# Kernel tuning notes

Hardware: AMD Instinct MI355X
Metric: run time of the kernel (lower is better)

Reference implementation:

```python
import jax, jax.numpy as jnp
import numpy as np
import math

N_HEADS = 8

def setup_inputs() -> dict:
    key = jax.random.key(0)
    ks = jax.random.split(key, 5)
    B, S, D = 2, 2048, 512
    return {
        "x": jax.random.normal(ks[0], (B, S, D), dtype=jnp.float32),
        "w_in": jax.random.normal(ks[1], (3 * D, D), dtype=jnp.float32) * (1.0 / math.sqrt(D)),
        "b_in": jax.random.normal(ks[2], (3 * D,), dtype=jnp.float32) * 0.01,
        "w_out": jax.random.normal(ks[3], (D, D), dtype=jnp.float32) * (1.0 / math.sqrt(D)),
        "b_out": jax.random.normal(ks[4], (D,), dtype=jnp.float32) * 0.01,
        "casual_mask": 1,
    }

def reference(x, w_in, b_in, w_out, b_out, casual_mask):
    B, S, D = x.shape
    H = N_HEADS
    dh = D // H
    # in_proj: torch Linear -> x @ W.T + b
    qvk = x @ w_in.T + b_in  # [B, S, 3D]
    # NOTE: source unpacks as q, v, k (chunk order quirk preserved)
    q, v, k = jnp.split(qvk, 3, axis=-1)
    # [B, S, D] -> [B, H, S, dh]
    def to_heads(t):
        return t.reshape(B, S, H, dh).transpose(0, 2, 1, 3)
    q, k, v = to_heads(q), to_heads(k), to_heads(v)
    scores = jnp.einsum("bhqd,bhkd->bhqk", q, k)  # [B, H, S, S]
    if casual_mask:
        # mask BEFORE scaling, as in the source (-inf unaffected by division)
        tri = jnp.triu(jnp.ones((S, S), dtype=bool), k=1)
        scores = jnp.where(tri, -jnp.inf, scores)
    scores = scores / math.sqrt(dh)
    attn = jax.nn.softmax(scores, axis=-1)
    out = jnp.einsum("bhqk,bhkd->bhqd", attn, v)  # [B, H, S, dh]
    out = out.transpose(0, 2, 1, 3).reshape(B, S, D)
    return out @ w_out.T + b_out
```

## Files before the change

### kernel.cpp

```cpp
#include <hip/hip_runtime.h>
#include <hip/hip_bf16.h>

typedef unsigned short u16;
typedef unsigned int u32;
typedef __attribute__((ext_vector_type(8))) short bf16x8;
typedef __attribute__((ext_vector_type(4))) short bf16x4;
typedef __attribute__((ext_vector_type(4))) float f32x4;

#define DEVI __device__ __forceinline__

DEVI u16 f2bf(float f) {
  union { float f; unsigned int u; } v; v.f = f;
  unsigned int u = v.u;
  unsigned int r = (u + 0x7fffu + ((u >> 16) & 1u)) >> 16;
  return (u16)r;
}

DEVI float bf2f(u16 b) {
  union { unsigned int u; float f; } v; v.u = ((unsigned int)b) << 16;
  return v.f;
}

DEVI float fexp2(float x) {
#if __has_builtin(__builtin_amdgcn_exp2f)
  return __builtin_amdgcn_exp2f(x);
#else
  return exp2f(x);
#endif
}

DEVI u32 pkbf(float a, float b) {
  union { float f; u32 u; } ua, ub;
  ua.f = a; ub.f = b;
  return __builtin_amdgcn_perm(ua.u + 0x8000u, ub.u + 0x8000u, 0x07060302u);
}

DEVI void lds_cp16(u16* lds, const u16* g) {
  __builtin_amdgcn_global_load_lds(
      (const __attribute__((address_space(1))) u32*)g,
      (__attribute__((address_space(3))) u32*)lds, 16, 0, 0);
}

DEVI f32x4 mfma16x16x16_bf16(bf16x4 a, bf16x4 b, f32x4 c) {
#if __has_builtin(__builtin_amdgcn_mfma_f32_16x16x16bf16_1k)
  return __builtin_amdgcn_mfma_f32_16x16x16bf16_1k(a, b, c, 0, 0, 0);
#else
  f32x4 d;
  asm volatile("v_mfma_f32_16x16x16_bf16 %0, %1, %2, %3"
               : "=v"(d) : "v"(a), "v"(b), "v"(c));
  return d;
#endif
}

__global__ __launch_bounds__(256) void cvt_all(
    const float4* __restrict__ x, const float4* __restrict__ wi,
    const float4* __restrict__ wo, u16* __restrict__ xb,
    u16* __restrict__ wib, u16* __restrict__ wob) {
  int i = blockIdx.x * 256 + threadIdx.x;
  const float4* src; u16* dst; int off;
  if (i < 524288)      { src = x;  dst = xb;  off = i; }
  else if (i < 720896) { src = wi; dst = wib; off = i - 524288; }
  else                 { src = wo; dst = wob; off = i - 720896; }
  float4 f = src[off];
  ushort4 o;
  o.x = f2bf(f.x); o.y = f2bf(f.y); o.z = f2bf(f.z); o.w = f2bf(f.w);
  ((ushort4*)dst)[off] = o;
}

__global__ __launch_bounds__(256) void inproj_gemm(
    const u16* __restrict__ xb, const u16* __restrict__ wb,
    const float* __restrict__ bin,
    u16* __restrict__ Qb, u16* __restrict__ Kb, u16* __restrict__ Vt) {
  const int K = 512;
  const float SCL = 0.180336878f;
  __shared__ u16 At[2][128 * 32];
  __shared__ u16 Bt[2][128 * 32];
  int tid = threadIdx.x;
  int w = tid >> 6, lane = tid & 63;
  int ql = lane & 15, quad = lane >> 4;
  int wr = w >> 1, wc = w & 1;
  int mtile = blockIdx.x * 128, ntile = blockIdx.y * 128;

  int r4 = lane >> 2, c4 = lane & 3;
  int swz4 = c4 ^ (r4 & 3);

  const u16* ag0 = xb + (size_t)(mtile + w * 32 + r4) * K + swz4 * 8;
  const u16* bg0 = wb + (size_t)(ntile + w * 32 + r4) * K + swz4 * 8;

  f32x4 acc[4][4];
#pragma unroll
  for (int t = 0; t < 4; ++t)
#pragma unroll
    for (int u = 0; u < 4; ++u) acc[t][u] = (f32x4){0, 0, 0, 0};

  lds_cp16(&At[0][w * 1024], ag0);
  lds_cp16(&At[0][w * 1024 + 512], ag0 + 16 * K);
  lds_cp16(&Bt[0][w * 1024], bg0);
  lds_cp16(&Bt[0][w * 1024 + 512], bg0 + 16 * K);

  int cb = ql & 3;
  for (int kk = 0; kk < 16; ++kk) {
    int cur = kk & 1;
    __syncthreads();
    if (kk < 15) {
      int k0 = (kk + 1) * 32;
      lds_cp16(&At[cur ^ 1][w * 1024], ag0 + k0);
      lds_cp16(&At[cur ^ 1][w * 1024 + 512], ag0 + 16 * K + k0);
      lds_cp16(&Bt[cur ^ 1][w * 1024], bg0 + k0);
      lds_cp16(&Bt[cur ^ 1][w * 1024 + 512], bg0 + 16 * K + k0);
    }
    bf16x8 af[4], bf[4];
#pragma unroll
    for (int t = 0; t < 4; ++t) {
      int row = wr * 64 + t * 16 + ql;
      af[t] = *(const bf16x8*)(&At[cur][row * 32 + ((quad ^ cb) * 8)]);
    }
#pragma unroll
    for (int u = 0; u < 4; ++u) {
      int row = wc * 64 + u * 16 + ql;
      bf[u] = *(const bf16x8*)(&Bt[cur][row * 32 + ((quad ^ cb) * 8)]);
    }
#pragma unroll
    for (int t = 0; t < 4; ++t)
#pragma unroll
      for (int u = 0; u < 4; ++u)
        acc[t][u] = __builtin_amdgcn_mfma_f32_16x16x32_bf16(af[t], bf[u], acc[t][u], 0, 0, 0);
  }

#pragma unroll
  for (int u = 0; u < 4; ++u) {
    int n = ntile + wc * 64 + u * 16 + ql;
    float bias = bin[n];
    int chunk = n >> 9;
    int nc = n & 511;
    int h = nc >> 6, d = nc & 63;
#pragma unroll
    for (int t = 0; t < 4; ++t)
#pragma unroll
      for (int r = 0; r < 4; ++r) {
        int m = mtile + wr * 64 + t * 16 + quad * 4 + r;
        int b = m >> 11, s = m & 2047;
        float v = acc[t][u][r] + bias;
        int bh = b * 8 + h;
        if (chunk == 0)      Qb[((size_t)bh * 2048 + s) * 64 + d] = f2bf(v * SCL);
        else if (chunk == 2) Kb[((size_t)bh * 2048 + s) * 64 + d] = f2bf(v);
        else                 Vt[((size_t)bh * 64 + d) * 2048 + s] = f2bf(v);
      }
  }
}

__global__ __launch_bounds__(256) void attn_kernel(
    const u16* __restrict__ Qb, const u16* __restrict__ Kb,
    const u16* __restrict__ Vt, u16* __restrict__ Pp, float* __restrict__ Ml) {
  const int S = 2048;
  __shared__ u16 Kt[2][4096];
  __shared__ u16 Vl[2][4096];
  int tid = threadIdx.x;
  int w = tid >> 6, lane = tid & 63;
  int ql = lane & 15, quad = lane >> 4;
  int j = blockIdx.x;
  int c = blockIdx.y;
  int bh = blockIdx.z;
  int tileA = j, tileB = 31 - j;
  int qbaseA = tileA * 64 + w * 16;
  int qbaseB = tileB * 64 + w * 16;
  const u16* Qh = Qb + (size_t)bh * S * 64;
  const u16* Kh = Kb + (size_t)bh * S * 64;
  const u16* Vh = Vt + (size_t)bh * 64 * S;

  int r8 = lane >> 3, c8 = lane & 7;
  int swz = c8 ^ r8;
  int cb = ql & 7;

  bf16x8 qA0 = *(const bf16x8*)(Qh + (size_t)(qbaseA + ql) * 64 + quad * 8);
  bf16x8 qA1 = *(const bf16x8*)(Qh + (size_t)(qbaseA + ql) * 64 + 32 + quad * 8);
  bf16x8 qB0 = *(const bf16x8*)(Qh + (size_t)(qbaseB + ql) * 64 + quad * 8);
  bf16x8 qB1 = *(const bf16x8*)(Qh + (size_t)(qbaseB + ql) * 64 + 32 + quad * 8);

  f32x4 oA[4] = {{0,0,0,0},{0,0,0,0},{0,0,0,0},{0,0,0,0}};
  f32x4 oB[4] = {{0,0,0,0},{0,0,0,0},{0,0,0,0},{0,0,0,0}};
  float lA = 0.0f, lB = 0.0f;

  auto kbOf = [&](int i) { return (i <= j) ? i : (i - j - 1); };
  auto stage = [&](int buf, int kbase) {
    const u16* kg = Kh + (size_t)(kbase + w * 16 + r8) * 64 + swz * 8;
    lds_cp16(&Kt[buf][w * 1024], kg);
    lds_cp16(&Kt[buf][w * 1024 + 512], kg + 8 * 64);
    const u16* vg = Vh + (size_t)(w * 16 + r8) * S + kbase + swz * 8;
    lds_cp16(&Vl[buf][w * 1024], vg);
    lds_cp16(&Vl[buf][w * 1024 + 512], vg + 8 * S);
  };
  auto process = [&](int cur, int kbase, int qbase, bf16x8 x0, bf16x8 x1,
                     f32x4 (&o)[4], float& l) {
    int q = qbase + ql;
    f32x4 st[4];
#pragma unroll
    for (int t = 0; t < 4; ++t) {
      const u16* kr = &Kt[cur][(t * 16 + ql) * 64];
      bf16x8 kf0 = *(const bf16x8*)(kr + ((quad ^ cb) * 8));
      bf16x8 kf1 = *(const bf16x8*)(kr + (((quad + 4) ^ cb) * 8));
      f32x4 s = {0, 0, 0, 0};
      s = __builtin_amdgcn_mfma_f32_16x16x32_bf16(kf0, x0, s, 0, 0, 0);
      s = __builtin_amdgcn_mfma_f32_16x16x32_bf16(kf1, x1, s, 0, 0, 0);
      st[t] = s;
    }
    bool needmask = (kbase + 63 > qbase);
    float e[4][4];
#pragma unroll
    for (int t = 0; t < 4; ++t)
#pragma unroll
      for (int r = 0; r < 4; ++r) {
        float v = st[t][r];
        if (needmask) {
          int key = kbase + t * 16 + quad * 4 + r;
          if (key > q) v = -3.0e38f;
        }
        e[t][r] = fexp2(v);
      }
    float s0 = (e[0][0] + e[0][1]) + (e[0][2] + e[0][3]);
    float s1 = (e[1][0] + e[1][1]) + (e[1][2] + e[1][3]);
    float s2 = (e[2][0] + e[2][1]) + (e[2][2] + e[2][3]);
    float s3 = (e[3][0] + e[3][1]) + (e[3][2] + e[3][3]);
    l += (s0 + s1) + (s2 + s3);
    bf16x4 p[4];
#pragma unroll
    for (int t = 0; t < 4; ++t) {
      union { bf16x4 v; u32 u[2]; } pk;
      pk.u[0] = pkbf(e[t][1], e[t][0]);
      pk.u[1] = pkbf(e[t][3], e[t][2]);
      p[t] = pk.v;
    }
#pragma unroll
    for (int t = 0; t < 4; ++t)
#pragma unroll
      for (int d = 0; d < 4; ++d) {
        const u16* vr = &Vl[cur][(d * 16 + ql) * 64];
        bf16x4 vf = *(const bf16x4*)(vr + (((t * 2 + (quad >> 1)) ^ cb) * 8 + (quad & 1) * 4));
        o[d] = mfma16x16x16_bf16(vf, p[t], o[d]);
      }
  };

  stage(0, kbOf(c * 11) * 64);

  for (int r = 0; r < 11; ++r) {
    int i = c * 11 + r;
    int cur = r & 1;
    __syncthreads();
    if (r < 10) stage(cur ^ 1, kbOf(i + 1) * 64);
    if (i <= j) process(cur, i * 64, qbaseA, qA0, qA1, oA, lA);
    else        process(cur, (i - j - 1) * 64, qbaseB, qB0, qB1, oB, lB);
  }

  lA += __shfl_xor(lA, 16); lA += __shfl_xor(lA, 32);
  lB += __shfl_xor(lB, 16); lB += __shfl_xor(lB, 32);
  int qrow = w * 16 + ql;
  size_t pb = ((((size_t)c * 16 + bh) * 16 + j) * 2) * 4096;
  size_t mb = ((((size_t)c * 16 + bh) * 16 + j) * 2) * 64;
  if (quad == 0) {
    Ml[mb + qrow]      = lA;
    Ml[mb + 64 + qrow] = lB;
  }
  bool validA = (c * 11 <= j);
  bool validB = (c * 11 + 10 > j);
  if (validA) {
#pragma unroll
    for (int dt = 0; dt < 4; ++dt) {
      ushort4 v;
      v.x = f2bf(oA[dt][0]); v.y = f2bf(oA[dt][1]);
      v.z = f2bf(oA[dt][2]); v.w = f2bf(oA[dt][3]);
      *(ushort4*)(Pp + pb + qrow * 64 + dt * 16 + quad * 4) = v;
    }
  }
  if (validB) {
#pragma unroll
    for (int dt = 0; dt < 4; ++dt) {
      ushort4 v;
      v.x = f2bf(oB[dt][0]); v.y = f2bf(oB[dt][1]);
      v.z = f2bf(oB[dt][2]); v.w = f2bf(oB[dt][3]);
      *(ushort4*)(Pp + pb + 4096 + qrow * 64 + dt * 16 + quad * 4) = v;
    }
  }
}

__global__ __launch_bounds__(256) void attn_merge(
    const u16* __restrict__ Pp, const float* __restrict__ Ml,
    u16* __restrict__ Ob) {
  int tid = threadIdx.x;
  int j = blockIdx.x, t = blockIdx.y, bh = blockIdx.z;
  int q = tid >> 2, ds = (tid & 3) * 16;
  float lc[3], L = 0.0f;
#pragma unroll
  for (int c = 0; c < 3; ++c) {
    lc[c] = Ml[((((size_t)c * 16 + bh) * 16 + j) * 2 + t) * 64 + q];
    L += lc[c];
  }
  float O[16];
#pragma unroll
  for (int i = 0; i < 16; ++i) O[i] = 0.0f;
#pragma unroll
  for (int c = 0; c < 3; ++c) {
    if (lc[c] > 0.0f) {
      size_t pb = ((((size_t)c * 16 + bh) * 16 + j) * 2 + t) * 4096 + q * 64 + ds;
      union { bf16x8 v; u16 e[8]; } a, b;
      a.v = *(const bf16x8*)(Pp + pb);
      b.v = *(const bf16x8*)(Pp + pb + 8);
#pragma unroll
      for (int i = 0; i < 8; ++i) {
        O[i]     += bf2f(a.e[i]);
        O[i + 8] += bf2f(b.e[i]);
      }
    }
  }
  float inv = 1.0f / L;
  int tile_abs = t ? (31 - j) : j;
  int s = tile_abs * 64 + q;
  int b2 = bh >> 3, h = bh & 7;
  size_t row = ((size_t)(b2 * 2048 + s)) * 512 + h * 64 + ds;
  union { bf16x8 v; u16 e[8]; } o0, o1;
#pragma unroll
  for (int i = 0; i < 8; ++i) {
    o0.e[i] = f2bf(O[i] * inv);
    o1.e[i] = f2bf(O[i + 8] * inv);
  }
  *(bf16x8*)(Ob + row)     = o0.v;
  *(bf16x8*)(Ob + row + 8) = o1.v;
}

__global__ __launch_bounds__(256) void outproj_gemm(
    const u16* __restrict__ Ob, const u16* __restrict__ wb,
    const float* __restrict__ bout, float* __restrict__ out) {
  const int K = 512;
  __shared__ u16 At[2][64 * 32];
  __shared__ u16 Bt[2][128 * 32];
  int tid = threadIdx.x;
  int w = tid >> 6, lane = tid & 63;
  int ql = lane & 15, quad = lane >> 4;
  int wr = w >> 1, wc = w & 1;
  int mtile = blockIdx.x * 64, ntile = blockIdx.y * 128;

  int r4 = lane >> 2, c4 = lane & 3;
  int swz4 = c4 ^ (r4 & 3);

  const u16* ag0 = Ob + (size_t)(mtile + w * 16 + r4) * K + swz4 * 8;
  const u16* bg0 = wb + (size_t)(ntile + w * 32 + r4) * K + swz4 * 8;

  f32x4 acc[2][4];
#pragma unroll
  for (int t = 0; t < 2; ++t)
#pragma unroll
    for (int u = 0; u < 4; ++u) acc[t][u] = (f32x4){0, 0, 0, 0};

  lds_cp16(&At[0][w * 512], ag0);
  lds_cp16(&Bt[0][w * 1024], bg0);
  lds_cp16(&Bt[0][w * 1024 + 512], bg0 + 16 * K);

  int cb = ql & 3;
  for (int kk = 0; kk < 16; ++kk) {
    int cur = kk & 1;
    __syncthreads();
    if (kk < 15) {
      int k0 = (kk + 1) * 32;
      lds_cp16(&At[cur ^ 1][w * 512], ag0 + k0);
      lds_cp16(&Bt[cur ^ 1][w * 1024], bg0 + k0);
      lds_cp16(&Bt[cur ^ 1][w * 1024 + 512], bg0 + 16 * K + k0);
    }
    bf16x8 af[2], bf[4];
#pragma unroll
    for (int t = 0; t < 2; ++t) {
      int row = wr * 32 + t * 16 + ql;
      af[t] = *(const bf16x8*)(&At[cur][row * 32 + ((quad ^ cb) * 8)]);
    }
#pragma unroll
    for (int u = 0; u < 4; ++u) {
      int row = wc * 64 + u * 16 + ql;
      bf[u] = *(const bf16x8*)(&Bt[cur][row * 32 + ((quad ^ cb) * 8)]);
    }
#pragma unroll
    for (int t = 0; t < 2; ++t)
#pragma unroll
      for (int u = 0; u < 4; ++u)
        acc[t][u] = __builtin_amdgcn_mfma_f32_16x16x32_bf16(af[t], bf[u], acc[t][u], 0, 0, 0);
  }

#pragma unroll
  for (int u = 0; u < 4; ++u) {
    int n = ntile + wc * 64 + u * 16 + ql;
    float bias = bout[n];
#pragma unroll
    for (int t = 0; t < 2; ++t)
#pragma unroll
      for (int r = 0; r < 4; ++r) {
        int mm = mtile + wr * 32 + t * 16 + quad * 4 + r;
        out[(size_t)mm * 512 + n] = acc[t][u][r] + bias;
      }
  }
}

extern "C" void kernel_launch(void* const* d_in, const int* in_sizes, int n_in,
                              void* d_out, int out_size, void* d_ws, size_t ws_size,
                              hipStream_t stream) {
  const float* x     = (const float*)d_in[0];
  const float* w_in  = (const float*)d_in[1];
  const float* b_in  = (const float*)d_in[2];
  const float* w_out = (const float*)d_in[3];
  const float* b_out = (const float*)d_in[4];
  float* out = (float*)d_out;
  char* ws = (char*)d_ws;

  u16* xb    = (u16*)(ws);
  u16* winb  = (u16*)(ws + 4194304);
  u16* woutb = (u16*)(ws + 5767168);
  u16* Qb    = (u16*)(ws + 6291456);
  u16* Kb    = (u16*)(ws + 10485760);
  u16* Vt    = (u16*)(ws + 14680064);
  u16* Ob    = (u16*)(ws + 18874368);
  u16* Pp    = (u16*)(ws + 23068672);
  float* Ml  = (float*)(ws + 35651584);

  cvt_all<<<3072, 256, 0, stream>>>((const float4*)x, (const float4*)w_in,
                                    (const float4*)w_out, xb, winb, woutb);
  inproj_gemm<<<dim3(32, 12), 256, 0, stream>>>(xb, winb, b_in, Qb, Kb, Vt);
  attn_kernel<<<dim3(16, 3, 16), 256, 0, stream>>>(Qb, Kb, Vt, Pp, Ml);
  attn_merge<<<dim3(16, 2, 16), 256, 0, stream>>>(Pp, Ml, Ob);
  outproj_gemm<<<dim3(64, 4), 256, 0, stream>>>(Ob, woutb, b_out, out);
}
```

Baseline: 131.1 us.

## Split attention work by key slice per wave and reduce partials through LDS

Each wave previously handled 16 query rows against the full 64-key block, reloading all K and V fragments from LDS. Now each wave takes a 16-key slice for all 64 query rows, which cuts per-wave LDS fragment reads, and the four waves' partial outputs and row sums are summed through a new shared-memory buffer in a flush step. The A and B tiles are now processed one after the other with a single accumulator set, which frees registers, and launch bounds now request 3 blocks per CU. The cost is extra LDS, extra barriers and the reduction work at each tile switch and at the end.

```diff
diff --git a/kernel.cpp b/kernel.cpp
--- a/kernel.cpp
+++ b/kernel.cpp
@@ -149,39 +149,50 @@
   }
 }
 
-__global__ __launch_bounds__(256) void attn_kernel(
+__global__ __launch_bounds__(256, 3) void attn_kernel(
     const u16* __restrict__ Qb, const u16* __restrict__ Kb,
     const u16* __restrict__ Vt, u16* __restrict__ Pp, float* __restrict__ Ml) {
   const int S = 2048;
   __shared__ u16 Kt[2][4096];
   __shared__ u16 Vl[2][4096];
+  __shared__ float Mg[64 * 66];
+  __shared__ float Lg[4][64];
   int tid = threadIdx.x;
   int w = tid >> 6, lane = tid & 63;
   int ql = lane & 15, quad = lane >> 4;
-  int j = blockIdx.x;
-  int c = blockIdx.y;
-  int bh = blockIdx.z;
+  int j = blockIdx.x, c = blockIdx.y, bh = blockIdx.z;
   int tileA = j, tileB = 31 - j;
-  int qbaseA = tileA * 64 + w * 16;
-  int qbaseB = tileB * 64 + w * 16;
   const u16* Qh = Qb + (size_t)bh * S * 64;
   const u16* Kh = Kb + (size_t)bh * S * 64;
   const u16* Vh = Vt + (size_t)bh * 64 * S;
-
   int r8 = lane >> 3, c8 = lane & 7;
   int swz = c8 ^ r8;
   int cb = ql & 7;
 
-  bf16x8 qA0 = *(const bf16x8*)(Qh + (size_t)(qbaseA + ql) * 64 + quad * 8);
-  bf16x8 qA1 = *(const bf16x8*)(Qh + (size_t)(qbaseA + ql) * 64 + 32 + quad * 8);
-  bf16x8 qB0 = *(const bf16x8*)(Qh + (size_t)(qbaseB + ql) * 64 + quad * 8);
-  bf16x8 qB1 = *(const bf16x8*)(Qh + (size_t)(qbaseB + ql) * 64 + 32 + quad * 8);
-
-  f32x4 oA[4] = {{0,0,0,0},{0,0,0,0},{0,0,0,0},{0,0,0,0}};
-  f32x4 oB[4] = {{0,0,0,0},{0,0,0,0},{0,0,0,0},{0,0,0,0}};
-  float lA = 0.0f, lB = 0.0f;
-
-  auto kbOf = [&](int i) { return (i <= j) ? i : (i - j - 1); };
+  int rsw = j + 1 - c * 11;
+  if (rsw < 0) rsw = 0;
+  if (rsw > 11) rsw = 11;
+
+  bf16x8 qf[4][2];
+  f32x4 o[4][4];
+  float l[4];
+
+  auto loadQ = [&](int tile) {
+    const u16* qp = Qh + (size_t)(tile * 64 + ql) * 64 + quad * 8;
+#pragma unroll
+    for (int qt = 0; qt < 4; ++qt) {
+      qf[qt][0] = *(const bf16x8*)(qp + qt * 1024);
+      qf[qt][1] = *(const bf16x8*)(qp + qt * 1024 + 32);
+    }
+  };
+  auto zeroAcc = [&]() {
+#pragma unroll
+    for (int dt = 0; dt < 4; ++dt)
+#pragma unroll
+      for (int qt = 0; qt < 4; ++qt) o[dt][qt] = (f32x4){0, 0, 0, 0};
+#pragma unroll
+    for (int qt = 0; qt < 4; ++qt) l[qt] = 0.0f;
+  };
   auto stage = [&](int buf, int kbase) {
     const u16* kg = Kh + (size_t)(kbase + w * 16 + r8) * 64 + swz * 8;
     lds_cp16(&Kt[buf][w * 1024], kg);
@@ -190,96 +201,125 @@
     lds_cp16(&Vl[buf][w * 1024], vg);
     lds_cp16(&Vl[buf][w * 1024 + 512], vg + 8 * S);
   };
-  auto process = [&](int cur, int kbase, int qbase, bf16x8 x0, bf16x8 x1,
-                     f32x4 (&o)[4], float& l) {
-    int q = qbase + ql;
-    f32x4 st[4];
-#pragma unroll
-    for (int t = 0; t < 4; ++t) {
-      const u16* kr = &Kt[cur][(t * 16 + ql) * 64];
-      bf16x8 kf0 = *(const bf16x8*)(kr + ((quad ^ cb) * 8));
-      bf16x8 kf1 = *(const bf16x8*)(kr + (((quad + 4) ^ cb) * 8));
-      f32x4 s = {0, 0, 0, 0};
-      s = __builtin_amdgcn_mfma_f32_16x16x32_bf16(kf0, x0, s, 0, 0, 0);
-      s = __builtin_amdgcn_mfma_f32_16x16x32_bf16(kf1, x1, s, 0, 0, 0);
-      st[t] = s;
-    }
-    bool needmask = (kbase + 63 > qbase);
+  auto process = [&](int cur, int kbase, int tile) {
+    const u16* kr = &Kt[cur][(w * 16 + ql) * 64];
+    bf16x8 kf0 = *(const bf16x8*)(kr + ((quad ^ cb) * 8));
+    bf16x8 kf1 = *(const bf16x8*)(kr + (((quad + 4) ^ cb) * 8));
+    f32x4 s[4];
+#pragma unroll
+    for (int qt = 0; qt < 4; ++qt) {
+      f32x4 t = {0, 0, 0, 0};
+      t = __builtin_amdgcn_mfma_f32_16x16x32_bf16(kf0, qf[qt][0], t, 0, 0, 0);
+      t = __builtin_amdgcn_mfma_f32_16x16x32_bf16(kf1, qf[qt][1], t, 0, 0, 0);
+      s[qt] = t;
+    }
+    bool needmask = (kbase == tile * 64);
     float e[4][4];
 #pragma unroll
-    for (int t = 0; t < 4; ++t)
+    for (int qt = 0; qt < 4; ++qt)
 #pragma unroll
       for (int r = 0; r < 4; ++r) {
-        float v = st[t][r];
+        float v = s[qt][r];
         if (needmask) {
-          int key = kbase + t * 16 + quad * 4 + r;
-          if (key > q) v = -3.0e38f;
+          int key = w * 16 + quad * 4 + r;
+          int qq = qt * 16 + ql;
+          if (key > qq) v = -3.0e38f;
         }
-        e[t][r] = fexp2(v);
+        e[qt][r] = fexp2(v);
       }
-    float s0 = (e[0][0] + e[0][1]) + (e[0][2] + e[0][3]);
-    float s1 = (e[1][0] + e[1][1]) + (e[1][2] + e[1][3]);
-    float s2 = (e[2][0] + e[2][1]) + (e[2][2] + e[2][3]);
-    float s3 = (e[3][0] + e[3][1]) + (e[3][2] + e[3][3]);
-    l += (s0 + s1) + (s2 + s3);
+#pragma unroll
+    for (int qt = 0; qt < 4; ++qt)
+      l[qt] += (e[qt][0] + e[qt][1]) + (e[qt][2] + e[qt][3]);
     bf16x4 p[4];
 #pragma unroll
-    for (int t = 0; t < 4; ++t) {
+    for (int qt = 0; qt < 4; ++qt) {
       union { bf16x4 v; u32 u[2]; } pk;
-      pk.u[0] = pkbf(e[t][1], e[t][0]);
-      pk.u[1] = pkbf(e[t][3], e[t][2]);
-      p[t] = pk.v;
-    }
-#pragma unroll
-    for (int t = 0; t < 4; ++t)
-#pragma unroll
-      for (int d = 0; d < 4; ++d) {
-        const u16* vr = &Vl[cur][(d * 16 + ql) * 64];
-        bf16x4 vf = *(const bf16x4*)(vr + (((t * 2 + (quad >> 1)) ^ cb) * 8 + (quad & 1) * 4));
-        o[d] = mfma16x16x16_bf16(vf, p[t], o[d]);
+      pk.u[0] = pkbf(e[qt][1], e[qt][0]);
+      pk.u[1] = pkbf(e[qt][3], e[qt][2]);
+      p[qt] = pk.v;
+    }
+#pragma unroll
+    for (int dt = 0; dt < 4; ++dt) {
+      const u16* vr = &Vl[cur][(dt * 16 + ql) * 64];
+      bf16x4 vf = *(const bf16x4*)(vr + (((w * 2 + (quad >> 1)) ^ cb) * 8 + (quad & 1) * 4));
+#pragma unroll
+      for (int qt = 0; qt < 4; ++qt)
+        o[dt][qt] = mfma16x16x16_bf16(vf, p[qt], o[dt][qt]);
+    }
+  };
+  auto flush = [&](int t01) {
+    float lv[4];
+#pragma unroll
+    for (int qt = 0; qt < 4; ++qt) {
+      float x = l[qt];
+      x += __shfl_xor(x, 16);
+      x += __shfl_xor(x, 32);
+      lv[qt] = x;
+    }
+    if (quad == 0) {
+#pragma unroll
+      for (int qt = 0; qt < 4; ++qt) Lg[w][qt * 16 + ql] = lv[qt];
+    }
+#pragma unroll
+    for (int st = 0; st < 4; ++st) {
+      __syncthreads();
+      int dt = (w + st) & 3;
+#pragma unroll
+      for (int qt = 0; qt < 4; ++qt) {
+        float* mg = &Mg[(qt * 16 + ql) * 66 + dt * 16 + quad * 4];
+        f32x4 val = o[dt][qt];
+        if (st) {
+          f32x4 old = *(const f32x4*)mg;
+          val = val + old;
+        }
+        *(f32x4*)mg = val;
       }
+    }
+    __syncthreads();
+    int q = tid >> 2, ds = (tid & 3) * 16;
+    size_t base = (((size_t)c * 16 + bh) * 16 + j) * 2 + t01;
+    if ((tid & 3) == 0)
+      Ml[base * 64 + q] = Lg[0][q] + Lg[1][q] + Lg[2][q] + Lg[3][q];
+    const float* mrow = &Mg[q * 66 + ds];
+    union { bf16x8 v; u16 e[8]; } o0, o1;
+#pragma unroll
+    for (int i = 0; i < 8; ++i) {
+      o0.e[i] = f2bf(mrow[i]);
+      o1.e[i] = f2bf(mrow[i + 8]);
+    }
+    u16* pp = Pp + base * 4096 + q * 64 + ds;
+    *(bf16x8*)pp = o0.v;
+    *(bf16x8*)(pp + 8) = o1.v;
+    __syncthreads();
   };
 
-  stage(0, kbOf(c * 11) * 64);
+  int i0 = c * 11;
+  int kb0 = (i0 <= j) ? i0 : (i0 - j - 1);
+  stage(0, kb0 * 64);
+  loadQ(rsw > 0 ? tileA : tileB);
+  zeroAcc();
 
   for (int r = 0; r < 11; ++r) {
-    int i = c * 11 + r;
     int cur = r & 1;
     __syncthreads();
-    if (r < 10) stage(cur ^ 1, kbOf(i + 1) * 64);
-    if (i <= j) process(cur, i * 64, qbaseA, qA0, qA1, oA, lA);
-    else        process(cur, (i - j - 1) * 64, qbaseB, qB0, qB1, oB, lB);
-  }
-
-  lA += __shfl_xor(lA, 16); lA += __shfl_xor(lA, 32);
-  lB += __shfl_xor(lB, 16); lB += __shfl_xor(lB, 32);
-  int qrow = w * 16 + ql;
-  size_t pb = ((((size_t)c * 16 + bh) * 16 + j) * 2) * 4096;
+    if (r == rsw && r > 0) {
+      flush(0);
+      loadQ(tileB);
+      zeroAcc();
+    }
+    if (r < 10) {
+      int i1 = c * 11 + r + 1;
+      int kb = (i1 <= j) ? i1 : (i1 - j - 1);
+      stage(cur ^ 1, kb * 64);
+    }
+    int i = c * 11 + r;
+    int kb = (i <= j) ? i : (i - j - 1);
+    process(cur, kb * 64, (r < rsw) ? tileA : tileB);
+  }
+  flush(rsw >= 11 ? 0 : 1);
   size_t mb = ((((size_t)c * 16 + bh) * 16 + j) * 2) * 64;
-  if (quad == 0) {
-    Ml[mb + qrow]      = lA;
-    Ml[mb + 64 + qrow] = lB;
-  }
-  bool validA = (c * 11 <= j);
-  bool validB = (c * 11 + 10 > j);
-  if (validA) {
-#pragma unroll
-    for (int dt = 0; dt < 4; ++dt) {
-      ushort4 v;
-      v.x = f2bf(oA[dt][0]); v.y = f2bf(oA[dt][1]);
-      v.z = f2bf(oA[dt][2]); v.w = f2bf(oA[dt][3]);
-      *(ushort4*)(Pp + pb + qrow * 64 + dt * 16 + quad * 4) = v;
-    }
-  }
-  if (validB) {
-#pragma unroll
-    for (int dt = 0; dt < 4; ++dt) {
-      ushort4 v;
-      v.x = f2bf(oB[dt][0]); v.y = f2bf(oB[dt][1]);
-      v.z = f2bf(oB[dt][2]); v.w = f2bf(oB[dt][3]);
-      *(ushort4*)(Pp + pb + 4096 + qrow * 64 + dt * 16 + quad * 4) = v;
-    }
-  }
+  if (rsw <= 0 && tid < 64) Ml[mb + tid] = 0.0f;
+  if (rsw >= 11 && tid < 64) Ml[mb + 64 + tid] = 0.0f;
 }
 
 __global__ __launch_bounds__(256) void attn_merge(
```

Result: slower. 222.5 us (+69.7%).
